# Performance work log

Measured on AMD Instinct MI355X. Metric: run time of the kernel, lower is better.

Reference implementation:

```python
import jax, jax.numpy as jnp
import numpy as np


def setup_inputs() -> dict:
    key = jax.random.key(0)
    k1, k2 = jax.random.split(key)
    query = jax.random.normal(k1, (16, 256, 32, 32), dtype=jnp.float32)
    search_map = jax.random.normal(k2, (16, 256, 64, 64), dtype=jnp.float32)
    return {"query": query, "search_map": search_map}


def reference(query, search_map):
    # query: [bs, c, h, w]; search_map: [bs, c, H, W]
    bs, c, h, w = query.shape
    # pad H and W by h//2, w//2 on each side (matches F.pad(left,right,top,bottom))
    padded = jnp.pad(search_map, ((0, 0), (0, 0), (h // 2, h // 2), (w // 2, w // 2)))

    def corr_one(map_, q_):
        # map_: [c, Hp, Wp], q_: [c, h, w]
        # per-sample cross-correlation: the query acts as a single-output conv kernel
        out = jax.lax.conv_general_dilated(
            map_[None],            # [1, c, Hp, Wp]
            q_[None],              # [1, c, h, w] -> OIHW
            window_strides=(1, 1),
            padding="VALID",
            dimension_numbers=("NCHW", "OIHW", "NCHW"),
        )
        return out[0]              # [1, Hout, Wout]

    # vmap over the batch: each sample uses its own query as the kernel
    return jax.vmap(corr_one)(padded, query)  # [bs, 1, Hout, Wout]
```

## Files before the change

kernel.cpp:

```cpp
#include <hip/hip_runtime.h>
#include <stdint.h>

typedef __bf16 bf16x8 __attribute__((ext_vector_type(8)));
typedef float  f32x4  __attribute__((ext_vector_type(4)));
typedef uint32_t u32x4 __attribute__((ext_vector_type(4)));

__device__ __forceinline__ uint16_t f2bf(float f) {
    uint32_t u = __builtin_bit_cast(uint32_t, f);
    u += 0x7FFFu + ((u >> 16) & 1u);
    return (uint16_t)(u >> 16);
}

__global__ __launch_bounds__(256) void qtrans_kernel(const float* __restrict__ Q,
                                                     uint16_t* __restrict__ Qt,
                                                     float* __restrict__ out) {
    __shared__ float T[8 * 1064];
    const int ch = blockIdx.x, b = blockIdx.y;
    const int tid = threadIdx.x;

    {
        int g = (b * 32 + ch) * 256 + tid;
        if (g < 67600) out[g] = 0.f;
    }

    const float* src = Q + ((size_t)(b * 256 + ch * 8)) * 1024;
    #pragma unroll
    for (int it = 0; it < 32; ++it) {
        int r = tid + it * 256;
        int c8 = r >> 10, rem = r & 1023;
        T[c8 * 1064 + (rem >> 5) * 33 + (rem & 31)] = src[(size_t)c8 * 1024 + rem];
    }
    __syncthreads();

    uint32_t* dst = (uint32_t*)Qt;
    #pragma unroll
    for (int it = 0; it < 16; ++it) {
        int o2 = tid + it * 256;
        int t  = (o2 & 3) * 2;
        int il = (o2 >> 2) & 15;
        int j  = (o2 >> 6) & 31;
        int ih = (o2 >> 11) & 1;
        float v0 = T[t * 1064 + (ih * 16 + il) * 33 + j];
        float v1 = T[(t + 1) * 1064 + (ih * 16 + il) * 33 + j];
        uint32_t pk = (uint32_t)f2bf(v0) | ((uint32_t)f2bf(v1) << 16);
        size_t oi = ((((size_t)(b * 2 + ih) * 32 + j) * 32 + ch) * 16 + il) * 4 + (t >> 1);
        dst[oi] = pk;
    }
}

__global__ __launch_bounds__(256, 4) void corr_kernel(const float* __restrict__ S,
                                                      const uint16_t* __restrict__ Qt,
                                                      float* __restrict__ out) {
    __shared__ __align__(16) char smem[40960];
    uint16_t* S_l = (uint16_t*)smem;
    float*    Pw  = (float*)smem;

    const int flat = blockIdx.x;
    const int b = ((flat & 7) << 1) | ((flat >> 9) & 1);
    const int d = (flat >> 3) & 63;
    const int tid = threadIdx.x, wave = tid >> 6, lane = tid & 63;
    const int l15 = lane & 15, l4 = lane >> 4;

    {
        const u32x4 z = {};
        for (int zi = tid; zi < 512; zi += 256) {
            int ch = zi >> 4, r = zi & 15;
            *(u32x4*)&S_l[ch * 640 + r * 8] = z;
        }
    }
    {
        const int sx = tid & 63, w = tid >> 6;
        const float* sp = S + ((size_t)b * 256) * 4096 + (size_t)d * 64;
        #pragma unroll
        for (int k = 0; k < 8; ++k) {
            int ch = w * 8 + k;
            float v[8];
            #pragma unroll
            for (int cc = 0; cc < 8; ++cc)
                v[cc] = sp[(size_t)(ch * 8 + cc) * 4096 + sx];
            u32x4 pk;
            #pragma unroll
            for (int q = 0; q < 4; ++q)
                pk[q] = (uint32_t)f2bf(v[2 * q]) | ((uint32_t)f2bf(v[2 * q + 1]) << 16);
            *(u32x4*)&S_l[ch * 640 + (sx + 16) * 8] = pk;
        }
    }
    __syncthreads();

    f32x4 acc[5][2] = {};

    #pragma unroll
    for (int jj = 0; jj < 4; ++jj) {
        const int j0a = wave + jj * 4;
        const uint16_t* qa0 = Qt + (((size_t)b * 2 + 0) * 32 + j0a) * 4096 + l4 * 128 + l15 * 8;
        const uint16_t* qa1 = Qt + (((size_t)b * 2 + 1) * 32 + j0a) * 4096 + l4 * 128 + l15 * 8;
        const uint16_t* qb0 = qa0 + 16 * 4096;
        const uint16_t* qb1 = qa1 + 16 * 4096;

        int rowt[5];
        #pragma unroll
        for (int t = 0; t < 5; ++t) {
            int rr = j0a + t * 16 + l15;
            rowt[t] = (rr < 80) ? rr : 0;
        }

        #pragma unroll
        for (int s = 0; s < 8; ++s) {
            bf16x8 Ba0 = *(const bf16x8*)(qa0 + s * 512);
            bf16x8 Ba1 = *(const bf16x8*)(qa1 + s * 512);
            bf16x8 Bb0 = *(const bf16x8*)(qb0 + s * 512);
            bf16x8 Bb1 = *(const bf16x8*)(qb1 + s * 512);
            const int chb = (s * 4 + l4) * 640;
            bf16x8 A[5];
            #pragma unroll
            for (int t = 0; t < 5; ++t)
                A[t] = *(const bf16x8*)&S_l[chb + rowt[t] * 8];
            #pragma unroll
            for (int t = 0; t < 5; ++t) {
                acc[t][0] = __builtin_amdgcn_mfma_f32_16x16x32_bf16(A[t], Ba0, acc[t][0], 0, 0, 0);
                acc[t][1] = __builtin_amdgcn_mfma_f32_16x16x32_bf16(A[t], Ba1, acc[t][1], 0, 0, 0);
            }
            #pragma unroll
            for (int t = 1; t < 5; ++t) {
                acc[t - 1][0] = __builtin_amdgcn_mfma_f32_16x16x32_bf16(A[t], Bb0, acc[t - 1][0], 0, 0, 0);
                acc[t - 1][1] = __builtin_amdgcn_mfma_f32_16x16x32_bf16(A[t], Bb1, acc[t - 1][1], 0, 0, 0);
            }
        }
    }

    __syncthreads();
    {
        float* pw = Pw + wave * 2560;
        #pragma unroll
        for (int m = 0; m < 5; ++m)
            #pragma unroll
            for (int n = 0; n < 2; ++n)
                *(f32x4*)&pw[(n * 16 + l15) * 80 + m * 16 + l4 * 4] = acc[m][n];
    }
    __syncthreads();
    for (int e = tid; e < 65 * 32; e += 256) {
        int x = e % 65, i = e / 65;
        int y = d - i + 16;
        if ((unsigned)y < 65u) {
            float v = Pw[0 * 2560 + i * 80 + x] + Pw[1 * 2560 + i * 80 + x]
                    + Pw[2 * 2560 + i * 80 + x] + Pw[3 * 2560 + i * 80 + x];
            atomicAdd(out + ((size_t)b * 4225 + (size_t)y * 65 + x), v);
        }
    }
}

__global__ __launch_bounds__(256) void naive_kernel(const float* __restrict__ Q,
                                                    const float* __restrict__ S,
                                                    float* __restrict__ out) {
    int gid = blockIdx.x * 256 + threadIdx.x;
    if (gid >= 67600) return;
    int b = gid / 4225, r = gid % 4225, y = r / 65, x = r % 65;
    int jlo = 16 - x; if (jlo < 0) jlo = 0;
    int jhi = 80 - x; if (jhi > 32) jhi = 32;
    float acc = 0.f;
    for (int c = 0; c < 256; ++c) {
        const float* Sb = S + ((size_t)(b * 256 + c)) * 4096;
        const float* Qb = Q + ((size_t)(b * 256 + c)) * 1024;
        for (int i = 0; i < 32; ++i) {
            int dd = y + i - 16;
            if ((unsigned)dd >= 64u) continue;
            const float* Sr = Sb + dd * 64 + (x - 16);
            const float* Qr = Qb + i * 32;
            for (int j = jlo; j < jhi; ++j) acc += Sr[j] * Qr[j];
        }
    }
    out[gid] = acc;
}

extern "C" void kernel_launch(void* const* d_in, const int* in_sizes, int n_in,
                              void* d_out, int out_size, void* d_ws, size_t ws_size,
                              hipStream_t stream) {
    (void)in_sizes; (void)n_in; (void)out_size;
    const float* Q = (const float*)d_in[0];
    const float* S = (const float*)d_in[1];
    float* out = (float*)d_out;

    const size_t QT_BYTES = (size_t)16 * 2 * 32 * 32 * 16 * 8 * 2;

    if (ws_size < QT_BYTES) {
        naive_kernel<<<(67600 + 255) / 256, 256, 0, stream>>>(Q, S, out);
        return;
    }
    uint16_t* Qt = (uint16_t*)d_ws;

    qtrans_kernel<<<dim3(32, 16), 256, 0, stream>>>(Q, Qt, out);
    corr_kernel<<<dim3(1024), 256, 0, stream>>>(S, Qt, out);
}
```

Baseline: 139.1 us.

## Split channels across blocks and process two output rows per block reusing Q fragments

Each block now processes two search-map rows over half of the channels instead of one row over all channels. The Q (B operand) fragments loaded from global memory are reused for both row tiles, halving Q reads per MFMA. In exchange, accumulators double and each block performs two reduction/atomicAdd epilogues, so more atomics hit the output. The batch-interleaving block swizzle is also replaced by a plain 3D grid.

Result: slower. 172.2 us (+23.8%).

```diff
diff --git a/kernel.cpp b/kernel.cpp
--- a/kernel.cpp
+++ b/kernel.cpp
@@ -55,45 +55,50 @@
     uint16_t* S_l = (uint16_t*)smem;
     float*    Pw  = (float*)smem;
 
-    const int flat = blockIdx.x;
-    const int b = ((flat & 7) << 1) | ((flat >> 9) & 1);
-    const int d = (flat >> 3) & 63;
+    const int half = blockIdx.x;
+    const int dp   = blockIdx.y;
+    const int b    = blockIdx.z;
     const int tid = threadIdx.x, wave = tid >> 6, lane = tid & 63;
     const int l15 = lane & 15, l4 = lane >> 4;
 
     {
         const u32x4 z = {};
         for (int zi = tid; zi < 512; zi += 256) {
-            int ch = zi >> 4, r = zi & 15;
-            *(u32x4*)&S_l[ch * 640 + r * 8] = z;
+            int t = zi >> 8, ch = (zi >> 4) & 15, r = zi & 15;
+            *(u32x4*)&S_l[t * 10240 + ch * 640 + r * 8] = z;
         }
     }
     {
         const int sx = tid & 63, w = tid >> 6;
-        const float* sp = S + ((size_t)b * 256) * 4096 + (size_t)d * 64;
+        const int tile = w >> 1;
+        const int chw  = (w & 1) * 8;
+        const int d    = dp * 2 + tile;
+        const float* sp = S + ((size_t)(b * 256 + half * 128)) * 4096 + (size_t)d * 64;
         #pragma unroll
         for (int k = 0; k < 8; ++k) {
-            int ch = w * 8 + k;
+            int chl = chw + k;
             float v[8];
             #pragma unroll
             for (int cc = 0; cc < 8; ++cc)
-                v[cc] = sp[(size_t)(ch * 8 + cc) * 4096 + sx];
+                v[cc] = sp[(size_t)(chl * 8 + cc) * 4096 + sx];
             u32x4 pk;
             #pragma unroll
             for (int q = 0; q < 4; ++q)
                 pk[q] = (uint32_t)f2bf(v[2 * q]) | ((uint32_t)f2bf(v[2 * q + 1]) << 16);
-            *(u32x4*)&S_l[ch * 640 + (sx + 16) * 8] = pk;
+            *(u32x4*)&S_l[tile * 10240 + chl * 640 + (sx + 16) * 8] = pk;
         }
     }
     __syncthreads();
 
-    f32x4 acc[5][2] = {};
+    f32x4 acc[2][5][2] = {};
 
     #pragma unroll
     for (int jj = 0; jj < 4; ++jj) {
         const int j0a = wave + jj * 4;
-        const uint16_t* qa0 = Qt + (((size_t)b * 2 + 0) * 32 + j0a) * 4096 + l4 * 128 + l15 * 8;
-        const uint16_t* qa1 = Qt + (((size_t)b * 2 + 1) * 32 + j0a) * 4096 + l4 * 128 + l15 * 8;
+        const uint16_t* qa0 = Qt + (((size_t)b * 2 + 0) * 32 + j0a) * 4096
+                                 + (half * 16 + l4) * 128 + l15 * 8;
+        const uint16_t* qa1 = Qt + (((size_t)b * 2 + 1) * 32 + j0a) * 4096
+                                 + (half * 16 + l4) * 128 + l15 * 8;
         const uint16_t* qb0 = qa0 + 16 * 4096;
         const uint16_t* qb1 = qa1 + 16 * 4096;
 
@@ -105,46 +110,54 @@
         }
 
         #pragma unroll
-        for (int s = 0; s < 8; ++s) {
+        for (int s = 0; s < 4; ++s) {
             bf16x8 Ba0 = *(const bf16x8*)(qa0 + s * 512);
             bf16x8 Ba1 = *(const bf16x8*)(qa1 + s * 512);
             bf16x8 Bb0 = *(const bf16x8*)(qb0 + s * 512);
             bf16x8 Bb1 = *(const bf16x8*)(qb1 + s * 512);
             const int chb = (s * 4 + l4) * 640;
-            bf16x8 A[5];
-            #pragma unroll
-            for (int t = 0; t < 5; ++t)
-                A[t] = *(const bf16x8*)&S_l[chb + rowt[t] * 8];
-            #pragma unroll
-            for (int t = 0; t < 5; ++t) {
-                acc[t][0] = __builtin_amdgcn_mfma_f32_16x16x32_bf16(A[t], Ba0, acc[t][0], 0, 0, 0);
-                acc[t][1] = __builtin_amdgcn_mfma_f32_16x16x32_bf16(A[t], Ba1, acc[t][1], 0, 0, 0);
+            #pragma unroll
+            for (int tile = 0; tile < 2; ++tile) {
+                const int tb = tile * 10240 + chb;
+                bf16x8 A[5];
+                #pragma unroll
+                for (int t = 0; t < 5; ++t)
+                    A[t] = *(const bf16x8*)&S_l[tb + rowt[t] * 8];
+                #pragma unroll
+                for (int t = 0; t < 5; ++t) {
+                    acc[tile][t][0] = __builtin_amdgcn_mfma_f32_16x16x32_bf16(A[t], Ba0, acc[tile][t][0], 0, 0, 0);
+                    acc[tile][t][1] = __builtin_amdgcn_mfma_f32_16x16x32_bf16(A[t], Ba1, acc[tile][t][1], 0, 0, 0);
+                }
+                #pragma unroll
+                for (int t = 1; t < 5; ++t) {
+                    acc[tile][t - 1][0] = __builtin_amdgcn_mfma_f32_16x16x32_bf16(A[t], Bb0, acc[tile][t - 1][0], 0, 0, 0);
+                    acc[tile][t - 1][1] = __builtin_amdgcn_mfma_f32_16x16x32_bf16(A[t], Bb1, acc[tile][t - 1][1], 0, 0, 0);
+                }
             }
-            #pragma unroll
-            for (int t = 1; t < 5; ++t) {
-                acc[t - 1][0] = __builtin_amdgcn_mfma_f32_16x16x32_bf16(A[t], Bb0, acc[t - 1][0], 0, 0, 0);
-                acc[t - 1][1] = __builtin_amdgcn_mfma_f32_16x16x32_bf16(A[t], Bb1, acc[t - 1][1], 0, 0, 0);
+        }
+    }
+
+    #pragma unroll
+    for (int tile = 0; tile < 2; ++tile) {
+        const int d = dp * 2 + tile;
+        __syncthreads();
+        {
+            float* pw = Pw + wave * 2560;
+            #pragma unroll
+            for (int m = 0; m < 5; ++m)
+                #pragma unroll
+                for (int n = 0; n < 2; ++n)
+                    *(f32x4*)&pw[(n * 16 + l15) * 80 + m * 16 + l4 * 4] = acc[tile][m][n];
+        }
+        __syncthreads();
+        for (int e = tid; e < 65 * 32; e += 256) {
+            int x = e % 65, i = e / 65;
+            int y = d - i + 16;
+            if ((unsigned)y < 65u) {
+                float v = Pw[0 * 2560 + i * 80 + x] + Pw[1 * 2560 + i * 80 + x]
+                        + Pw[2 * 2560 + i * 80 + x] + Pw[3 * 2560 + i * 80 + x];
+                atomicAdd(out + ((size_t)b * 4225 + (size_t)y * 65 + x), v);
             }
-        }
-    }
-
-    __syncthreads();
-    {
-        float* pw = Pw + wave * 2560;
-        #pragma unroll
-        for (int m = 0; m < 5; ++m)
-            #pragma unroll
-            for (int n = 0; n < 2; ++n)
-                *(f32x4*)&pw[(n * 16 + l15) * 80 + m * 16 + l4 * 4] = acc[m][n];
-    }
-    __syncthreads();
-    for (int e = tid; e < 65 * 32; e += 256) {
-        int x = e % 65, i = e / 65;
-        int y = d - i + 16;
-        if ((unsigned)y < 65u) {
-            float v = Pw[0 * 2560 + i * 80 + x] + Pw[1 * 2560 + i * 80 + x]
-                    + Pw[2 * 2560 + i * 80 + x] + Pw[3 * 2560 + i * 80 + x];
-            atomicAdd(out + ((size_t)b * 4225 + (size_t)y * 65 + x), v);
         }
     }
 }
@@ -189,5 +202,5 @@
     uint16_t* Qt = (uint16_t*)d_ws;
 
     qtrans_kernel<<<dim3(32, 16), 256, 0, stream>>>(Q, Qt, out);
-    corr_kernel<<<dim3(1024), 256, 0, stream>>>(S, Qt, out);
-}
+    corr_kernel<<<dim3(2, 32, 16), 256, 0, stream>>>(S, Qt, out);
+}
```
